# Kernel optimization log

Hardware: AMD Instinct MI355X
Metric: run time of the kernel (lower is better)

## Reference

```python
import jax, jax.numpy as jnp
import numpy as np

N_NODES = 50000
N_EDGES = 1280000
N_GRAPHS = 64
IN_CH = 6
HID = 64
SLOPE = 0.2  # LeakyReLU negative slope


def _lrelu(x):
    return jax.nn.leaky_relu(x, SLOPE)


def _edge_conv(x, src, dst, W1, b1, W2, b2):
    # PyG EdgeConv: message = nn([x_i, x_j - x_i]); x_i = x[dst], x_j = x[src]; max-aggr onto dst
    xi = x[dst]                                   # [E, F]
    m = jnp.concatenate([xi, x[src] - xi], -1)    # [E, 2F]
    h = _lrelu(_lrelu(m @ W1 + b1) @ W2 + b2)     # [E, H]
    agg = jax.ops.segment_max(h, dst, num_segments=N_NODES)
    return jnp.where(jnp.isneginf(agg), 0.0, agg)  # nodes with no in-edges -> 0


def setup_inputs() -> dict:
    key = jax.random.key(0)
    ks = jax.random.split(key, 12)
    glorot = lambda k, fi, fo: jax.random.normal(k, (fi, fo), jnp.float32) * np.sqrt(2.0 / (fi + fo))
    x = jax.random.normal(ks[0], (N_NODES, IN_CH), jnp.float32)
    edge_index = jax.random.randint(ks[1], (2, N_EDGES), 0, N_NODES, jnp.int64 if jax.config.x64_enabled else jnp.int32)
    batch = jnp.sort(jax.random.randint(ks[2], (N_NODES,), 0, N_GRAPHS))
    return {
        "x": x, "edge_index": edge_index, "batch": batch,
        "W1": glorot(ks[3], 2 * IN_CH, HID), "b1": jnp.zeros((HID,), jnp.float32),
        "W2": glorot(ks[4], HID, HID),       "b2": jnp.zeros((HID,), jnp.float32),
        "W3": glorot(ks[5], 2 * HID, HID),   "b3": jnp.zeros((HID,), jnp.float32),
        "W4": glorot(ks[6], HID, HID),       "b4": jnp.zeros((HID,), jnp.float32),
        "Wc1": glorot(ks[7], 2 * HID, HID),  "bc1": jnp.zeros((HID,), jnp.float32),
        "Wc2": glorot(ks[8], HID, 1),        "bc2": jnp.zeros((1,), jnp.float32),
    }


def reference(x, edge_index, batch, W1, b1, W2, b2, W3, b3, W4, b4, Wc1, bc1, Wc2, bc2):
    src, dst = edge_index[0], edge_index[1]
    h = _edge_conv(x, src, dst, W1, b1, W2, b2)   # [N, H]
    h = _edge_conv(h, src, dst, W3, b3, W4, b4)   # [N, H]
    # global mean + max pool per graph
    cnt = jax.ops.segment_sum(jnp.ones((N_NODES,), h.dtype), batch, num_segments=N_GRAPHS)
    mean_p = jax.ops.segment_sum(h, batch, num_segments=N_GRAPHS) / jnp.clip(cnt, 1.0)[:, None]
    max_p = jax.ops.segment_max(h, batch, num_segments=N_GRAPHS)
    max_p = jnp.where(jnp.isneginf(max_p), 0.0, max_p)
    g = jnp.concatenate([mean_p, max_p], -1)      # [G, 2H]
    logits = _lrelu(g @ Wc1 + bc1) @ Wc2 + bc2    # dropout is identity at inference
    return logits.squeeze(-1)                      # [G]
```

## Files before the change

### kernel.cpp

```cpp
#include <hip/hip_runtime.h>
#include <hip/hip_bf16.h>

#define SLOPE 0.2f
#define NPB 64
#define CAP 2048
#define MAXBUCK 1024
#define EPB 4096
#define XF1B 512
#define PPARTS 16

typedef _Float16 f16x8  __attribute__((ext_vector_type(8)));
typedef float    f32x4  __attribute__((ext_vector_type(4)));
typedef unsigned u32;
typedef unsigned u32x4  __attribute__((ext_vector_type(4)));

__device__ __forceinline__ float lrelu(float v) { return fmaxf(v, SLOPE * v); }

__device__ __forceinline__ float lane_bcast(float v, int k) {
    return __int_as_float(__builtin_amdgcn_readlane(__float_as_int(v), k));
}

__device__ __forceinline__ f16x8 lrelu8(f16x8 v) {
    f16x8 s = v * (_Float16)SLOPE;
#if __has_builtin(__builtin_elementwise_max)
    return __builtin_elementwise_max(v, s);
#else
    f16x8 r;
#pragma unroll
    for (int i = 0; i < 8; ++i) r[i] = v[i] > s[i] ? v[i] : s[i];
    return r;
#endif
}

__device__ __forceinline__ void split_f16(float v, _Float16& h, _Float16& l) {
    h = (_Float16)v;
    l = (_Float16)(v - (float)h);
}
__device__ __forceinline__ u32 pack_f16(_Float16 a, _Float16 b) {
    return (u32)__builtin_bit_cast(unsigned short, a) |
           ((u32)__builtin_bit_cast(unsigned short, b) << 16);
}

__global__ void __launch_bounds__(256) scatter_xform1_kernel(
    const int* __restrict__ srcI, const int* __restrict__ dstI,
    int* __restrict__ cursor, u32* __restrict__ pairW,
    int E, int nNodes, int nBuck, int nCntB,
    const float* __restrict__ x,
    const float* __restrict__ W1, const float* __restrict__ b1,
    _Float16* __restrict__ Ph, _Float16* __restrict__ Qh)
{
    if (blockIdx.x < nCntB) {
        __shared__ int cnt[MAXBUCK];
        __shared__ int base[MAXBUCK];
        const int tid = threadIdx.x;
        const int e0 = blockIdx.x * EPB;
        const int e1 = min(e0 + EPB, E);

        for (int b = tid; b < nBuck; b += 256) cnt[b] = 0;
        __syncthreads();
        for (int e = e0 + tid; e < e1; e += 256)
            atomicAdd(&cnt[dstI[e] >> 6], 1);
        __syncthreads();
        for (int b = tid; b < nBuck; b += 256) {
            int c = cnt[b];
            base[b] = (c > 0) ? (b * CAP + atomicAdd(&cursor[b], c)) : 0;
            cnt[b] = 0;
        }
        __syncthreads();
        for (int e = e0 + tid; e < e1; e += 256) {
            const int d = dstI[e];
            const int b = d >> 6;
            const int loc = atomicAdd(&cnt[b], 1);
            const int pos = min(base[b] + loc, b * CAP + CAP - 1);
            pairW[pos] = ((u32)srcI[e] << 6) | (u32)(d & (NPB - 1));
        }
        return;
    }
    const int lane = threadIdx.x & 63;
    const int wave = ((blockIdx.x - nCntB) * 256 + threadIdx.x) >> 6;
    const int nw   = (XF1B * 256) >> 6;

    float wd[6], wb[6];
#pragma unroll
    for (int r = 0; r < 6; ++r) {
        wb[r] = W1[(6 + r) * 64 + lane];
        wd[r] = W1[r * 64 + lane] - wb[r];
    }
    const float bb = b1[lane];
    for (int i = wave; i < nNodes; i += nw) {
        const float* xr = x + (size_t)i * 6;
        float p = bb, q = 0.f;
#pragma unroll
        for (int r = 0; r < 6; ++r) {
            float xv = xr[r];
            p = fmaf(xv, wd[r], p);
            q = fmaf(xv, wb[r], q);
        }
        Ph[(size_t)i * 64 + lane] = (_Float16)p;
        Qh[(size_t)i * 64 + lane] = (_Float16)q;
    }
}

__global__ void __launch_bounds__(256) bucket_sort_kernel(
    const u32* __restrict__ pairW, const int* __restrict__ cursor,
    int2* __restrict__ rowInfo, int* __restrict__ sortedSrc, int nNodes)
{
    __shared__ int nodeCnt[NPB];
    __shared__ int nodeCur[NPB];
    const int b   = blockIdx.x;
    const int n0  = b * NPB;
    const int n1  = min(n0 + NPB, nNodes);
    const int tid = threadIdx.x;
    if (tid < NPB) nodeCnt[tid] = 0;
    __syncthreads();
    const int r0 = b * CAP;
    const int r1 = r0 + min(cursor[b], CAP);
    for (int i = r0 + tid; i < r1; i += 256)
        atomicAdd(&nodeCnt[pairW[i] & (NPB - 1)], 1);
    __syncthreads();
    if (tid < 64) {
        const int c = nodeCnt[tid];
        int inc = c;
#pragma unroll
        for (int off = 1; off < 64; off <<= 1) {
            int t = __shfl_up(inc, off);
            if (tid >= off) inc += t;
        }
        const int st = r0 + inc - c;
        nodeCur[tid] = st;
        if (tid < n1 - n0) rowInfo[n0 + tid] = make_int2(st, c);
    }
    __syncthreads();
    for (int i = r0 + tid; i < r1; i += 256) {
        const u32 w = pairW[i];
        const int pos = atomicAdd(&nodeCur[w & (NPB - 1)], 1);
        sortedSrc[pos] = (int)(w >> 6);
    }
}

__global__ void __launch_bounds__(256) node_xform2_kernel(
    const float* __restrict__ A,
    const float* __restrict__ W3, const float* __restrict__ b3,
    _Float16* __restrict__ Ph, _Float16* __restrict__ Qh, int nNodes)
{
    const int lane = threadIdx.x & 63;
    const int wave = (blockIdx.x * blockDim.x + threadIdx.x) >> 6;
    const int nw   = (gridDim.x * blockDim.x) >> 6;

    float wd[64], wb[64];
#pragma unroll
    for (int k = 0; k < 64; ++k) {
        wb[k] = W3[(64 + k) * 64 + lane];
        wd[k] = W3[k * 64 + lane] - wb[k];
    }
    const float bb = b3[lane];

    for (int i = wave; i < nNodes; i += nw) {
        const float a = A[(size_t)i * 64 + lane];
        float p0 = bb, p1 = 0.f, p2 = 0.f, p3 = 0.f;
        float q0 = 0.f, q1 = 0.f, q2 = 0.f, q3 = 0.f;
#pragma unroll
        for (int k = 0; k < 64; k += 4) {
            float a0 = lane_bcast(a, k);
            float a1 = lane_bcast(a, k + 1);
            float a2 = lane_bcast(a, k + 2);
            float a3 = lane_bcast(a, k + 3);
            p0 = fmaf(a0, wd[k],     p0);  q0 = fmaf(a0, wb[k],     q0);
            p1 = fmaf(a1, wd[k + 1], p1);  q1 = fmaf(a1, wb[k + 1], q1);
            p2 = fmaf(a2, wd[k + 2], p2);  q2 = fmaf(a2, wb[k + 2], q2);
            p3 = fmaf(a3, wd[k + 3], p3);  q3 = fmaf(a3, wb[k + 3], q3);
        }
        Ph[(size_t)i * 64 + lane] = (_Float16)((p0 + p1) + (p2 + p3));
        Qh[(size_t)i * 64 + lane] = (_Float16)((q0 + q1) + (q2 + q3));
    }
}

__global__ void __launch_bounds__(256) edge_agg_mfma_kernel(
    const _Float16* __restrict__ Ph, const _Float16* __restrict__ Qh,
    const int2* __restrict__ rowInfo, const int* __restrict__ sortedSrc,
    const float* __restrict__ W, const float* __restrict__ b,
    float* __restrict__ outB, int nNodes)
{
    __shared__ u32x4 wlds[16][64];

    const int tid  = threadIdx.x;
    const int lane = tid & 63;
    const int cn   = lane & 15;
    const int q    = lane >> 4;
    const int wv   = tid >> 6;
    const int wave = (blockIdx.x * 256 + tid) >> 6;
    const int nw   = (gridDim.x * 256) >> 6;

#pragma unroll
    for (int i = 0; i < 4; ++i) {
        const int f    = wv + i * 4;
        const int isLo = f >> 3;
        const int g    = f & 7;
        const int nt   = g >> 1;
        const int ks   = g & 1;
        u32x4 d;
#pragma unroll
        for (int p = 0; p < 4; ++p) {
            float w0 = W[(ks * 32 + q * 8 + 2 * p)     * 64 + nt * 16 + cn];
            float w1 = W[(ks * 32 + q * 8 + 2 * p + 1) * 64 + nt * 16 + cn];
            _Float16 h0, l0, h1, l1;
            split_f16(w0, h0, l0);
            split_f16(w1, h1, l1);
            d[p] = isLo ? pack_f16(l0, l1) : pack_f16(h0, h1);
        }
        wlds[f][lane] = d;
    }
    float bc[4];
#pragma unroll
    for (int nt = 0; nt < 4; ++nt) bc[nt] = b[nt * 16 + cn];
    __syncthreads();

    const u32 nClamp = (u32)(nNodes - 1);

    for (int base = wave; base < nNodes; base += 2 * nw) {
        const int n1 = base;
        const int n2 = base + nw;
        const bool has2 = (n2 < nNodes);

        const int2 ri1 = rowInfo[n1];
        const int2 ri2 = has2 ? rowInfo[n2] : make_int2(ri1.x, 0);
        const int rs1  = __builtin_amdgcn_readfirstlane(ri1.x);
        const int deg1 = __builtin_amdgcn_readfirstlane(ri1.y);
        const int rs2  = __builtin_amdgcn_readfirstlane(ri2.x);
        const int deg2 = __builtin_amdgcn_readfirstlane(ri2.y);
        const int d1c = max(deg1, 1) - 1;
        const int d2c = max(deg2, 1) - 1;

        const f16x8* P1 = (const f16x8*)(Ph + (size_t)n1 * 64);
        const f16x8* P2 = (const f16x8*)(Ph + (size_t)(has2 ? n2 : n1) * 64);
        const f16x8 p1A = P1[q], p1B = P1[4 + q];
        const f16x8 p2A = P2[q], p2B = P2[4 + q];

        float m10 = -INFINITY, m11 = -INFINITY, m12 = -INFINITY, m13 = -INFINITY;
        float m20 = -INFINITY, m21 = -INFINITY, m22 = -INFINITY, m23 = -INFINITY;

        const int gmax = max(deg1, deg2);
        for (int g0 = 0; g0 < gmax; g0 += 32) {
            u32 sA1 = (u32)sortedSrc[rs1 + min(g0 + cn,      d1c)];
            u32 sB1 = (u32)sortedSrc[rs1 + min(g0 + 16 + cn, d1c)];
            u32 sA2 = (u32)sortedSrc[rs2 + min(g0 + cn,      d2c)];
            u32 sB2 = (u32)sortedSrc[rs2 + min(g0 + 16 + cn, d2c)];
            sA1 = min(sA1, nClamp); sB1 = min(sB1, nClamp);
            sA2 = min(sA2, nClamp); sB2 = min(sB2, nClamp);
            const f16x8* QA1 = (const f16x8*)(Qh + (size_t)sA1 * 64);
            const f16x8* QB1 = (const f16x8*)(Qh + (size_t)sB1 * 64);
            const f16x8* QA2 = (const f16x8*)(Qh + (size_t)sA2 * 64);
            const f16x8* QB2 = (const f16x8*)(Qh + (size_t)sB2 * 64);
            const f16x8 qA1a = QA1[q], qA1b = QA1[4 + q];
            const f16x8 qB1a = QB1[q], qB1b = QB1[4 + q];
            const f16x8 qA2a = QA2[q], qA2b = QA2[4 + q];
            const f16x8 qB2a = QB2[q], qB2b = QB2[4 + q];

            if (g0 < deg1) {
                const f16x8 A00 = lrelu8(p1A + qA1a);
                const f16x8 A01 = lrelu8(p1B + qA1b);
                const f16x8 A10 = lrelu8(p1A + qB1a);
                const f16x8 A11 = lrelu8(p1B + qB1b);
#pragma unroll
                for (int nt = 0; nt < 4; ++nt) {
                    const f16x8 wh0 = __builtin_bit_cast(f16x8, wlds[nt * 2][lane]);
                    const f16x8 wh1 = __builtin_bit_cast(f16x8, wlds[nt * 2 + 1][lane]);
                    const f16x8 wl0 = __builtin_bit_cast(f16x8, wlds[8 + nt * 2][lane]);
                    const f16x8 wl1 = __builtin_bit_cast(f16x8, wlds[8 + nt * 2 + 1][lane]);
                    f32x4 a; a[0] = a[1] = a[2] = a[3] = bc[nt];
                    a = __builtin_amdgcn_mfma_f32_16x16x32_f16(A00, wl0, a, 0, 0, 0);
                    a = __builtin_amdgcn_mfma_f32_16x16x32_f16(A00, wh0, a, 0, 0, 0);
                    a = __builtin_amdgcn_mfma_f32_16x16x32_f16(A01, wl1, a, 0, 0, 0);
                    a = __builtin_amdgcn_mfma_f32_16x16x32_f16(A01, wh1, a, 0, 0, 0);
                    f32x4 c; c[0] = c[1] = c[2] = c[3] = bc[nt];
                    c = __builtin_amdgcn_mfma_f32_16x16x32_f16(A10, wl0, c, 0, 0, 0);
                    c = __builtin_amdgcn_mfma_f32_16x16x32_f16(A10, wh0, c, 0, 0, 0);
                    c = __builtin_amdgcn_mfma_f32_16x16x32_f16(A11, wl1, c, 0, 0, 0);
                    c = __builtin_amdgcn_mfma_f32_16x16x32_f16(A11, wh1, c, 0, 0, 0);
                    float m = (nt == 0) ? m10 : (nt == 1) ? m11 : (nt == 2) ? m12 : m13;
                    m = fmaxf(m, fmaxf(fmaxf(a[0], a[1]), fmaxf(a[2], a[3])));
                    m = fmaxf(m, fmaxf(fmaxf(c[0], c[1]), fmaxf(c[2], c[3])));
                    if (nt == 0) m10 = m; else if (nt == 1) m11 = m;
                    else if (nt == 2) m12 = m; else m13 = m;
                }
            }
            if (g0 < deg2) {
                const f16x8 A00 = lrelu8(p2A + qA2a);
                const f16x8 A01 = lrelu8(p2B + qA2b);
                const f16x8 A10 = lrelu8(p2A + qB2a);
                const f16x8 A11 = lrelu8(p2B + qB2b);
#pragma unroll
                for (int nt = 0; nt < 4; ++nt) {
                    const f16x8 wh0 = __builtin_bit_cast(f16x8, wlds[nt * 2][lane]);
                    const f16x8 wh1 = __builtin_bit_cast(f16x8, wlds[nt * 2 + 1][lane]);
                    const f16x8 wl0 = __builtin_bit_cast(f16x8, wlds[8 + nt * 2][lane]);
                    const f16x8 wl1 = __builtin_bit_cast(f16x8, wlds[8 + nt * 2 + 1][lane]);
                    f32x4 a; a[0] = a[1] = a[2] = a[3] = bc[nt];
                    a = __builtin_amdgcn_mfma_f32_16x16x32_f16(A00, wl0, a, 0, 0, 0);
                    a = __builtin_amdgcn_mfma_f32_16x16x32_f16(A00, wh0, a, 0, 0, 0);
                    a = __builtin_amdgcn_mfma_f32_16x16x32_f16(A01, wl1, a, 0, 0, 0);
                    a = __builtin_amdgcn_mfma_f32_16x16x32_f16(A01, wh1, a, 0, 0, 0);
                    f32x4 c; c[0] = c[1] = c[2] = c[3] = bc[nt];
                    c = __builtin_amdgcn_mfma_f32_16x16x32_f16(A10, wl0, c, 0, 0, 0);
                    c = __builtin_amdgcn_mfma_f32_16x16x32_f16(A10, wh0, c, 0, 0, 0);
                    c = __builtin_amdgcn_mfma_f32_16x16x32_f16(A11, wl1, c, 0, 0, 0);
                    c = __builtin_amdgcn_mfma_f32_16x16x32_f16(A11, wh1, c, 0, 0, 0);
                    float m = (nt == 0) ? m20 : (nt == 1) ? m21 : (nt == 2) ? m22 : m23;
                    m = fmaxf(m, fmaxf(fmaxf(a[0], a[1]), fmaxf(a[2], a[3])));
                    m = fmaxf(m, fmaxf(fmaxf(c[0], c[1]), fmaxf(c[2], c[3])));
                    if (nt == 0) m20 = m; else if (nt == 1) m21 = m;
                    else if (nt == 2) m22 = m; else m23 = m;
                }
            }
        }

        m10 = fmaxf(m10, __shfl_xor(m10, 16)); m10 = fmaxf(m10, __shfl_xor(m10, 32));
        m11 = fmaxf(m11, __shfl_xor(m11, 16)); m11 = fmaxf(m11, __shfl_xor(m11, 32));
        m12 = fmaxf(m12, __shfl_xor(m12, 16)); m12 = fmaxf(m12, __shfl_xor(m12, 32));
        m13 = fmaxf(m13, __shfl_xor(m13, 16)); m13 = fmaxf(m13, __shfl_xor(m13, 32));
        float sel1 = (q < 2) ? ((q == 0) ? m10 : m11) : ((q == 2) ? m12 : m13);
        outB[(size_t)n1 * 64 + q * 16 + cn] = (deg1 > 0) ? lrelu(sel1) : 0.0f;

        if (has2) {
            m20 = fmaxf(m20, __shfl_xor(m20, 16)); m20 = fmaxf(m20, __shfl_xor(m20, 32));
            m21 = fmaxf(m21, __shfl_xor(m21, 16)); m21 = fmaxf(m21, __shfl_xor(m21, 32));
            m22 = fmaxf(m22, __shfl_xor(m22, 16)); m22 = fmaxf(m22, __shfl_xor(m22, 32));
            m23 = fmaxf(m23, __shfl_xor(m23, 16)); m23 = fmaxf(m23, __shfl_xor(m23, 32));
            float sel2 = (q < 2) ? ((q == 0) ? m20 : m21) : ((q == 2) ? m22 : m23);
            outB[(size_t)n2 * 64 + q * 16 + cn] = (deg2 > 0) ? lrelu(sel2) : 0.0f;
        }
    }
}

__device__ __forceinline__ int lower_bound_i(const int* __restrict__ a, int n, int key)
{
    int lo = 0, hi = n;
    while (lo < hi) {
        int mid = (lo + hi) >> 1;
        if (a[mid] < key) lo = mid + 1; else hi = mid;
    }
    return lo;
}

__global__ void __launch_bounds__(256) pool_kernel(
    const float* __restrict__ B, const int* __restrict__ batch,
    float* __restrict__ gpart, int nNodes)
{
    const int gid  = blockIdx.x / PPARTS;
    const int part = blockIdx.x % PPARTS;
    const int c    = threadIdx.x & 63;
    const int wid  = threadIdx.x >> 6;

    const int s = lower_bound_i(batch, nNodes, gid);
    const int e = lower_bound_i(batch, nNodes, gid + 1);
    const int len = e - s;
    const int ps = s + (len * part) / PPARTS;
    const int pe = s + (len * (part + 1)) / PPARTS;

    float sum = 0.f, mx = -INFINITY;
    for (int n = ps + wid; n < pe; n += 4) {
        float v = B[(size_t)n * 64 + c];
        sum += v;
        mx = fmaxf(mx, v);
    }
    __shared__ float ssum[4][64];
    __shared__ float smax[4][64];
    ssum[wid][c] = sum;
    smax[wid][c] = mx;
    __syncthreads();
    if (wid == 0) {
        sum = (ssum[0][c] + ssum[1][c]) + (ssum[2][c] + ssum[3][c]);
        mx  = fmaxf(fmaxf(smax[0][c], smax[1][c]), fmaxf(smax[2][c], smax[3][c]));
        float* row = gpart + (size_t)blockIdx.x * 132;
        row[c]      = sum;
        row[64 + c] = mx;
        if (c == 0) row[128] = (float)(pe - ps);
    }
}

__global__ void __launch_bounds__(64) cls_kernel(
    const float* __restrict__ gpart,
    const float* __restrict__ Wc1, const float* __restrict__ bc1,
    const float* __restrict__ Wc2, const float* __restrict__ bc2,
    float* __restrict__ out)
{
    __shared__ float g[128];
    const int gid = blockIdx.x;
    const int c   = threadIdx.x;

    float s = 0.f, m = -INFINITY, cnt = 0.f;
#pragma unroll
    for (int p = 0; p < PPARTS; ++p) {
        const float* row = gpart + (size_t)(gid * PPARTS + p) * 132;
        s += row[c];
        m = fmaxf(m, row[64 + c]);
        cnt += row[128];
    }
    g[c]      = s / fmaxf(cnt, 1.0f);
    g[64 + c] = (cnt > 0.f) ? m : 0.0f;
    __syncthreads();

    float t = bc1[c];
#pragma unroll 8
    for (int k = 0; k < 128; ++k) t = fmaf(g[k], Wc1[k * 64 + c], t);
    t = lrelu(t);
    float p = t * Wc2[c];
#pragma unroll
    for (int off = 32; off > 0; off >>= 1) p += __shfl_down(p, off);
    if (c == 0) out[gid] = p + bc2[0];
}

static inline size_t align_up(size_t v, size_t a) { return (v + a - 1) & ~(a - 1); }

extern "C" void kernel_launch(void* const* d_in, const int* in_sizes, int n_in,
                              void* d_out, int out_size, void* d_ws, size_t ws_size,
                              hipStream_t stream)
{
    const float* x     = (const float*)d_in[0];
    const int*   ei    = (const int*)d_in[1];
    const int*   batch = (const int*)d_in[2];
    const float* W1  = (const float*)d_in[3];
    const float* b1  = (const float*)d_in[4];
    const float* W2  = (const float*)d_in[5];
    const float* b2  = (const float*)d_in[6];
    const float* W3  = (const float*)d_in[7];
    const float* b3  = (const float*)d_in[8];
    const float* W4  = (const float*)d_in[9];
    const float* b4  = (const float*)d_in[10];
    const float* Wc1 = (const float*)d_in[11];
    const float* bc1 = (const float*)d_in[12];
    const float* Wc2 = (const float*)d_in[13];
    const float* bc2 = (const float*)d_in[14];
    float* out = (float*)d_out;

    const int nNodes  = in_sizes[0] / 6;
    const int E       = in_sizes[1] / 2;
    const int nGraphs = out_size;
    const int* srcI = ei;
    const int* dstI = ei + E;
    const int nBuck = (nNodes + NPB - 1) / NPB;
    const int nCntB = (E + EPB - 1) / EPB;

    char* wsp = (char*)d_ws;
    size_t off = 0;
    int*  cursor    = (int*)(wsp + off);   off = align_up(off + (size_t)MAXBUCK * 4, 256);
    int2* rowInfo   = (int2*)(wsp + off);  off = align_up(off + (size_t)nNodes * 8, 256);
    int*  sortedSrc = (int*)(wsp + off);   off = align_up(off + (size_t)nBuck * CAP * 4, 256);
    u32*  pairW     = (u32*)(wsp + off);   off = align_up(off + (size_t)nBuck * CAP * 4, 256);
    const size_t nFeat = (size_t)nNodes * 64;
    _Float16* Ph   = (_Float16*)(wsp + off);  off = align_up(off + nFeat * 2, 256);
    _Float16* Qh   = (_Float16*)(wsp + off);  off = align_up(off + nFeat * 2, 256);
    float*    B1   = (float*)(wsp + off);     off = align_up(off + nFeat * 4, 256);
    float*    B2   = (float*)(wsp + off);     off = align_up(off + nFeat * 4, 256);
    float*    gpart= (float*)(wsp + off);     off = align_up(off + (size_t)nGraphs * PPARTS * 132 * 4, 256);
    (void)ws_size;

    (void)hipMemsetAsync(cursor, 0, (size_t)nBuck * 4, stream);
    scatter_xform1_kernel<<<nCntB + XF1B, 256, 0, stream>>>(
        srcI, dstI, cursor, pairW, E, nNodes, nBuck, nCntB, x, W1, b1, Ph, Qh);
    bucket_sort_kernel<<<nBuck, 256, 0, stream>>>(pairW, cursor, rowInfo,
                                                  sortedSrc, nNodes);

    edge_agg_mfma_kernel<<<2048, 256, 0, stream>>>(Ph, Qh, rowInfo, sortedSrc,
                                                   W2, b2, B1, nNodes);
    node_xform2_kernel<<<2048, 256, 0, stream>>>(B1, W3, b3, Ph, Qh, nNodes);
    edge_agg_mfma_kernel<<<2048, 256, 0, stream>>>(Ph, Qh, rowInfo, sortedSrc,
                                                   W4, b4, B2, nNodes);

    pool_kernel<<<nGraphs * PPARTS, 256, 0, stream>>>(B2, batch, gpart, nNodes);
    cls_kernel<<<nGraphs, 64, 0, stream>>>(gpart, Wc1, bc1, Wc2, bc2, out);
}
```

Measured before the change: 274.2 us.

## Use MFMA for second node transform, store activations in fp16, fuse pool and classifier

The second-layer node transform moves from per-lane FMA with readlane broadcasts to 16x16x32 f16 MFMA, using a hi/lo split of the weights staged in LDS. Intermediate node features B1/B2 are now stored as fp16 instead of fp32, halving their traffic. The pool and classifier kernels are merged through a last-block-done atomic counter, removing one launch. The scatter kernel caches edge indices in registers to avoid re-reading them, and EPB is halved to give more blocks. Storing features in fp16 adds rounding error, and the atomic completion pattern depends on the memset of the done counters.

```diff
diff --git a/kernel.cpp b/kernel.cpp
--- a/kernel.cpp
+++ b/kernel.cpp
@@ -5,7 +5,7 @@
 #define NPB 64
 #define CAP 2048
 #define MAXBUCK 1024
-#define EPB 4096
+#define EPB 2048
 #define XF1B 512
 #define PPARTS 16
 
@@ -58,8 +58,16 @@
 
         for (int b = tid; b < nBuck; b += 256) cnt[b] = 0;
         __syncthreads();
-        for (int e = e0 + tid; e < e1; e += 256)
-            atomicAdd(&cnt[dstI[e] >> 6], 1);
+        int dreg[EPB / 256], sreg[EPB / 256];
+#pragma unroll
+        for (int i = 0; i < EPB / 256; ++i) {
+            const int e = e0 + tid + i * 256;
+            if (e < e1) {
+                dreg[i] = dstI[e];
+                sreg[i] = srcI[e];
+                atomicAdd(&cnt[dreg[i] >> 6], 1);
+            }
+        }
         __syncthreads();
         for (int b = tid; b < nBuck; b += 256) {
             int c = cnt[b];
@@ -67,12 +75,16 @@
             cnt[b] = 0;
         }
         __syncthreads();
-        for (int e = e0 + tid; e < e1; e += 256) {
-            const int d = dstI[e];
-            const int b = d >> 6;
-            const int loc = atomicAdd(&cnt[b], 1);
-            const int pos = min(base[b] + loc, b * CAP + CAP - 1);
-            pairW[pos] = ((u32)srcI[e] << 6) | (u32)(d & (NPB - 1));
+#pragma unroll
+        for (int i = 0; i < EPB / 256; ++i) {
+            const int e = e0 + tid + i * 256;
+            if (e < e1) {
+                const int d = dreg[i];
+                const int b = d >> 6;
+                const int loc = atomicAdd(&cnt[b], 1);
+                const int pos = min(base[b] + loc, b * CAP + CAP - 1);
+                pairW[pos] = ((u32)sreg[i] << 6) | (u32)(d & (NPB - 1));
+            }
         }
         return;
     }
@@ -138,40 +150,80 @@
     }
 }
 
-__global__ void __launch_bounds__(256) node_xform2_kernel(
-    const float* __restrict__ A,
+__global__ void __launch_bounds__(256) node_xform2_mfma_kernel(
+    const _Float16* __restrict__ B1h,
     const float* __restrict__ W3, const float* __restrict__ b3,
     _Float16* __restrict__ Ph, _Float16* __restrict__ Qh, int nNodes)
 {
-    const int lane = threadIdx.x & 63;
-    const int wave = (blockIdx.x * blockDim.x + threadIdx.x) >> 6;
-    const int nw   = (gridDim.x * blockDim.x) >> 6;
-
-    float wd[64], wb[64];
-#pragma unroll
-    for (int k = 0; k < 64; ++k) {
-        wb[k] = W3[(64 + k) * 64 + lane];
-        wd[k] = W3[k * 64 + lane] - wb[k];
-    }
-    const float bb = b3[lane];
-
-    for (int i = wave; i < nNodes; i += nw) {
-        const float a = A[(size_t)i * 64 + lane];
-        float p0 = bb, p1 = 0.f, p2 = 0.f, p3 = 0.f;
-        float q0 = 0.f, q1 = 0.f, q2 = 0.f, q3 = 0.f;
-#pragma unroll
-        for (int k = 0; k < 64; k += 4) {
-            float a0 = lane_bcast(a, k);
-            float a1 = lane_bcast(a, k + 1);
-            float a2 = lane_bcast(a, k + 2);
-            float a3 = lane_bcast(a, k + 3);
-            p0 = fmaf(a0, wd[k],     p0);  q0 = fmaf(a0, wb[k],     q0);
-            p1 = fmaf(a1, wd[k + 1], p1);  q1 = fmaf(a1, wb[k + 1], q1);
-            p2 = fmaf(a2, wd[k + 2], p2);  q2 = fmaf(a2, wb[k + 2], q2);
-            p3 = fmaf(a3, wd[k + 3], p3);  q3 = fmaf(a3, wb[k + 3], q3);
-        }
-        Ph[(size_t)i * 64 + lane] = (_Float16)((p0 + p1) + (p2 + p3));
-        Qh[(size_t)i * 64 + lane] = (_Float16)((q0 + q1) + (q2 + q3));
+    __shared__ u32x4 wlds[32][64];
+    const int tid  = threadIdx.x;
+    const int lane = tid & 63;
+    const int cn   = lane & 15;
+    const int q    = lane >> 4;
+    const int wv   = tid >> 6;
+
+#pragma unroll
+    for (int i = 0; i < 8; ++i) {
+        const int f    = wv + i * 4;
+        const int out  = f >> 2;
+        const int ks   = (f >> 1) & 1;
+        const int isLo = f & 1;
+        const int n    = (out & 3) * 16 + cn;
+        u32x4 d;
+#pragma unroll
+        for (int p = 0; p < 4; ++p) {
+            const int k = ks * 32 + q * 8 + 2 * p;
+            float w0, w1;
+            if (out < 4) {
+                w0 = W3[k * 64 + n]       - W3[(64 + k) * 64 + n];
+                w1 = W3[(k + 1) * 64 + n] - W3[(65 + k) * 64 + n];
+            } else {
+                w0 = W3[(64 + k) * 64 + n];
+                w1 = W3[(65 + k) * 64 + n];
+            }
+            _Float16 h0, l0, h1, l1;
+            split_f16(w0, h0, l0);
+            split_f16(w1, h1, l1);
+            d[p] = isLo ? pack_f16(l0, l1) : pack_f16(h0, h1);
+        }
+        wlds[f][lane] = d;
+    }
+    float bc[4];
+#pragma unroll
+    for (int nt = 0; nt < 4; ++nt) bc[nt] = b3[nt * 16 + cn];
+    __syncthreads();
+
+    const int nTiles = (nNodes + 15) >> 4;
+    const int wave = (blockIdx.x * 256 + tid) >> 6;
+    const int nw   = (gridDim.x * 256) >> 6;
+
+    for (int t = wave; t < nTiles; t += nw) {
+        const int n0 = t * 16;
+        const int node = min(n0 + cn, nNodes - 1);
+        const f16x8* Ar = (const f16x8*)(B1h + (size_t)node * 64);
+        const f16x8 aA = Ar[q], aB = Ar[4 + q];
+
+#pragma unroll
+        for (int out = 0; out < 8; ++out) {
+            const f16x8 wh0 = __builtin_bit_cast(f16x8, wlds[out * 4 + 0][lane]);
+            const f16x8 wl0 = __builtin_bit_cast(f16x8, wlds[out * 4 + 1][lane]);
+            const f16x8 wh1 = __builtin_bit_cast(f16x8, wlds[out * 4 + 2][lane]);
+            const f16x8 wl1 = __builtin_bit_cast(f16x8, wlds[out * 4 + 3][lane]);
+            f32x4 a;
+            const float init = (out < 4) ? bc[out & 3] : 0.0f;
+            a[0] = a[1] = a[2] = a[3] = init;
+            a = __builtin_amdgcn_mfma_f32_16x16x32_f16(aA, wl0, a, 0, 0, 0);
+            a = __builtin_amdgcn_mfma_f32_16x16x32_f16(aA, wh0, a, 0, 0, 0);
+            a = __builtin_amdgcn_mfma_f32_16x16x32_f16(aB, wl1, a, 0, 0, 0);
+            a = __builtin_amdgcn_mfma_f32_16x16x32_f16(aB, wh1, a, 0, 0, 0);
+            _Float16* dst = (out < 4) ? Ph : Qh;
+            const int col = (out & 3) * 16 + cn;
+#pragma unroll
+            for (int j = 0; j < 4; ++j) {
+                const int nn = n0 + q * 4 + j;
+                if (nn < nNodes) dst[(size_t)nn * 64 + col] = (_Float16)a[j];
+            }
+        }
     }
 }
 
@@ -179,7 +231,7 @@
     const _Float16* __restrict__ Ph, const _Float16* __restrict__ Qh,
     const int2* __restrict__ rowInfo, const int* __restrict__ sortedSrc,
     const float* __restrict__ W, const float* __restrict__ b,
-    float* __restrict__ outB, int nNodes)
+    _Float16* __restrict__ outB, int nNodes)
 {
     __shared__ u32x4 wlds[16][64];
 
@@ -319,7 +371,8 @@
         m12 = fmaxf(m12, __shfl_xor(m12, 16)); m12 = fmaxf(m12, __shfl_xor(m12, 32));
         m13 = fmaxf(m13, __shfl_xor(m13, 16)); m13 = fmaxf(m13, __shfl_xor(m13, 32));
         float sel1 = (q < 2) ? ((q == 0) ? m10 : m11) : ((q == 2) ? m12 : m13);
-        outB[(size_t)n1 * 64 + q * 16 + cn] = (deg1 > 0) ? lrelu(sel1) : 0.0f;
+        outB[(size_t)n1 * 64 + q * 16 + cn] =
+            (_Float16)((deg1 > 0) ? lrelu(sel1) : 0.0f);
 
         if (has2) {
             m20 = fmaxf(m20, __shfl_xor(m20, 16)); m20 = fmaxf(m20, __shfl_xor(m20, 32));
@@ -327,7 +380,8 @@
             m22 = fmaxf(m22, __shfl_xor(m22, 16)); m22 = fmaxf(m22, __shfl_xor(m22, 32));
             m23 = fmaxf(m23, __shfl_xor(m23, 16)); m23 = fmaxf(m23, __shfl_xor(m23, 32));
             float sel2 = (q < 2) ? ((q == 0) ? m20 : m21) : ((q == 2) ? m22 : m23);
-            outB[(size_t)n2 * 64 + q * 16 + cn] = (deg2 > 0) ? lrelu(sel2) : 0.0f;
+            outB[(size_t)n2 * 64 + q * 16 + cn] =
+                (_Float16)((deg2 > 0) ? lrelu(sel2) : 0.0f);
         }
     }
 }
@@ -342,14 +396,18 @@
     return lo;
 }
 
-__global__ void __launch_bounds__(256) pool_kernel(
-    const float* __restrict__ B, const int* __restrict__ batch,
-    float* __restrict__ gpart, int nNodes)
+__global__ void __launch_bounds__(256) pool_cls_kernel(
+    const _Float16* __restrict__ Bh, const int* __restrict__ batch,
+    float* __restrict__ gpart, int* __restrict__ done,
+    const float* __restrict__ Wc1, const float* __restrict__ bc1,
+    const float* __restrict__ Wc2, const float* __restrict__ bc2,
+    float* __restrict__ out, int nNodes)
 {
     const int gid  = blockIdx.x / PPARTS;
     const int part = blockIdx.x % PPARTS;
     const int c    = threadIdx.x & 63;
     const int wid  = threadIdx.x >> 6;
+    const int tid  = threadIdx.x;
 
     const int s = lower_bound_i(batch, nNodes, gid);
     const int e = lower_bound_i(batch, nNodes, gid + 1);
@@ -359,12 +417,13 @@
 
     float sum = 0.f, mx = -INFINITY;
     for (int n = ps + wid; n < pe; n += 4) {
-        float v = B[(size_t)n * 64 + c];
+        float v = (float)Bh[(size_t)n * 64 + c];
         sum += v;
         mx = fmaxf(mx, v);
     }
     __shared__ float ssum[4][64];
     __shared__ float smax[4][64];
+    __shared__ int lastFlag;
     ssum[wid][c] = sum;
     smax[wid][c] = mx;
     __syncthreads();
@@ -375,39 +434,35 @@
         row[c]      = sum;
         row[64 + c] = mx;
         if (c == 0) row[128] = (float)(pe - ps);
-    }
-}
-
-__global__ void __launch_bounds__(64) cls_kernel(
-    const float* __restrict__ gpart,
-    const float* __restrict__ Wc1, const float* __restrict__ bc1,
-    const float* __restrict__ Wc2, const float* __restrict__ bc2,
-    float* __restrict__ out)
-{
-    __shared__ float g[128];
-    const int gid = blockIdx.x;
-    const int c   = threadIdx.x;
-
-    float s = 0.f, m = -INFINITY, cnt = 0.f;
-#pragma unroll
-    for (int p = 0; p < PPARTS; ++p) {
-        const float* row = gpart + (size_t)(gid * PPARTS + p) * 132;
-        s += row[c];
-        m = fmaxf(m, row[64 + c]);
-        cnt += row[128];
-    }
-    g[c]      = s / fmaxf(cnt, 1.0f);
-    g[64 + c] = (cnt > 0.f) ? m : 0.0f;
-    __syncthreads();
-
-    float t = bc1[c];
+        __threadfence();
+    }
+    __syncthreads();
+    if (tid == 0)
+        lastFlag = (atomicAdd(&done[gid], 1) == PPARTS - 1) ? 1 : 0;
+    __syncthreads();
+    if (lastFlag && wid == 0) {
+        __threadfence();
+        __shared__ float g[128];
+        float ss = 0.f, m = -INFINITY, cnt = 0.f;
+#pragma unroll
+        for (int p = 0; p < PPARTS; ++p) {
+            const float* row = gpart + (size_t)(gid * PPARTS + p) * 132;
+            ss += row[c];
+            m = fmaxf(m, row[64 + c]);
+            cnt += row[128];
+        }
+        g[c]      = ss / fmaxf(cnt, 1.0f);
+        g[64 + c] = (cnt > 0.f) ? m : 0.0f;
+        __builtin_amdgcn_s_barrier();
+        float t = bc1[c];
 #pragma unroll 8
-    for (int k = 0; k < 128; ++k) t = fmaf(g[k], Wc1[k * 64 + c], t);
-    t = lrelu(t);
-    float p = t * Wc2[c];
-#pragma unroll
-    for (int off = 32; off > 0; off >>= 1) p += __shfl_down(p, off);
-    if (c == 0) out[gid] = p + bc2[0];
+        for (int k = 0; k < 128; ++k) t = fmaf(g[k], Wc1[k * 64 + c], t);
+        t = lrelu(t);
+        float p = t * Wc2[c];
+#pragma unroll
+        for (int off = 32; off > 0; off >>= 1) p += __shfl_down(p, off);
+        if (c == 0) out[gid] = p + bc2[0];
+    }
 }
 
 static inline size_t align_up(size_t v, size_t a) { return (v + a - 1) & ~(a - 1); }
@@ -443,30 +498,31 @@
 
     char* wsp = (char*)d_ws;
     size_t off = 0;
-    int*  cursor    = (int*)(wsp + off);   off = align_up(off + (size_t)MAXBUCK * 4, 256);
+    int*  cursor    = (int*)(wsp + off);   off += (size_t)MAXBUCK * 4;
+    int*  done      = (int*)(wsp + off);   off = align_up(off + 256 * 4, 256);
     int2* rowInfo   = (int2*)(wsp + off);  off = align_up(off + (size_t)nNodes * 8, 256);
     int*  sortedSrc = (int*)(wsp + off);   off = align_up(off + (size_t)nBuck * CAP * 4, 256);
     u32*  pairW     = (u32*)(wsp + off);   off = align_up(off + (size_t)nBuck * CAP * 4, 256);
     const size_t nFeat = (size_t)nNodes * 64;
     _Float16* Ph   = (_Float16*)(wsp + off);  off = align_up(off + nFeat * 2, 256);
     _Float16* Qh   = (_Float16*)(wsp + off);  off = align_up(off + nFeat * 2, 256);
-    float*    B1   = (float*)(wsp + off);     off = align_up(off + nFeat * 4, 256);
-    float*    B2   = (float*)(wsp + off);     off = align_up(off + nFeat * 4, 256);
+    _Float16* B1h  = (_Float16*)(wsp + off);  off = align_up(off + nFeat * 2, 256);
+    _Float16* B2h  = (_Float16*)(wsp + off);  off = align_up(off + nFeat * 2, 256);
     float*    gpart= (float*)(wsp + off);     off = align_up(off + (size_t)nGraphs * PPARTS * 132 * 4, 256);
     (void)ws_size;
 
-    (void)hipMemsetAsync(cursor, 0, (size_t)nBuck * 4, stream);
+    (void)hipMemsetAsync(cursor, 0, (size_t)(MAXBUCK + 256) * 4, stream);
     scatter_xform1_kernel<<<nCntB + XF1B, 256, 0, stream>>>(
         srcI, dstI, cursor, pairW, E, nNodes, nBuck, nCntB, x, W1, b1, Ph, Qh);
     bucket_sort_kernel<<<nBuck, 256, 0, stream>>>(pairW, cursor, rowInfo,
                                                   sortedSrc, nNodes);
 
     edge_agg_mfma_kernel<<<2048, 256, 0, stream>>>(Ph, Qh, rowInfo, sortedSrc,
-                                                   W2, b2, B1, nNodes);
-    node_xform2_kernel<<<2048, 256, 0, stream>>>(B1, W3, b3, Ph, Qh, nNodes);
+                                                   W2, b2, B1h, nNodes);
+    node_xform2_mfma_kernel<<<1024, 256, 0, stream>>>(B1h, W3, b3, Ph, Qh, nNodes);
     edge_agg_mfma_kernel<<<2048, 256, 0, stream>>>(Ph, Qh, rowInfo, sortedSrc,
-                                                   W4, b4, B2, nNodes);
-
-    pool_kernel<<<nGraphs * PPARTS, 256, 0, stream>>>(B2, batch, gpart, nNodes);
-    cls_kernel<<<nGraphs, 64, 0, stream>>>(gpart, Wc1, bc1, Wc2, bc2, out);
-}
+                                                   W4, b4, B2h, nNodes);
+
+    pool_cls_kernel<<<nGraphs * PPARTS, 256, 0, stream>>>(
+        B2h, batch, gpart, done, Wc1, bc1, Wc2, bc2, out, nNodes);
+}
```

Measured after the change: 284.2 us. 1.04x slower.
